# Kernel optimization log

Measured on AMD Instinct MI355X. Metric: run time of the kernel, lower is better.

## Reference

```python
import jax, jax.numpy as jnp
import numpy as np

EPS = 1e-3  # Keras LayerNormalization default epsilon


def setup_inputs() -> dict:
    key = jax.random.key(0)
    ks = jax.random.split(key, 10)
    B, S, D, U = 4, 4096, 1024, 1024
    sc_in = 1.0 / np.sqrt(D)
    sc_u = 1.0 / np.sqrt(U)
    return {
        "inputs": jax.random.normal(ks[0], (B, S, D), dtype=jnp.float32),
        "w1": jax.random.normal(ks[1], (D, U), dtype=jnp.float32) * sc_in,
        "b1": jnp.zeros((U,), dtype=jnp.float32),
        "w2": jax.random.normal(ks[2], (U, U), dtype=jnp.float32) * sc_u,
        "b2": jnp.zeros((U,), dtype=jnp.float32),
        "wg": jax.random.normal(ks[3], (D, U), dtype=jnp.float32) * sc_in,
        "bg": jnp.zeros((U,), dtype=jnp.float32),
        "ws": jax.random.normal(ks[4], (D, U), dtype=jnp.float32) * sc_in,
        "bs": jnp.zeros((U,), dtype=jnp.float32),
        "gamma": jnp.ones((U,), dtype=jnp.float32),
        "beta": jnp.zeros((U,), dtype=jnp.float32),
    }


def reference(inputs, w1, b1, w2, b2, wg, bg, ws, bs, gamma, beta):
    # hidden branch: Dense(relu) -> (dropout inactive at inference) -> Dense
    h = jax.nn.relu(jnp.einsum('bsd,du->bsu', inputs, w1) + b1)
    x = jnp.einsum('bsu,uv->bsv', h, w2) + b2
    # gate on raw inputs
    g = jax.nn.sigmoid(jnp.einsum('bsd,du->bsu', inputs, wg) + bg)
    # skip projection
    s = jnp.einsum('bsd,du->bsu', inputs, ws) + bs
    y = x * g + s
    # LayerNormalization over last axis (Keras default eps=1e-3)
    mu = jnp.mean(y, axis=-1, keepdims=True)
    var = jnp.mean(jnp.square(y - mu), axis=-1, keepdims=True)
    return (y - mu) * jax.lax.rsqrt(var + EPS) * gamma + beta
```

## Files before the change

kernel.cpp:

```cpp
#include <hip/hip_runtime.h>
#include <hip/hip_bf16.h>

typedef short short8 __attribute__((ext_vector_type(8)));
typedef float f32x4 __attribute__((ext_vector_type(4)));

#define M_TOT 16384
#define NDIM  1024
#define BM 256
#define BN 256
#define BK 64
#define KH 32
#define NT (NDIM / BK)

static __device__ __forceinline__ unsigned short f2bf(float f) {
  unsigned int u = __builtin_bit_cast(unsigned int, f);
  unsigned int r = (u + 0x7fffu + ((u >> 16) & 1u)) >> 16;
  return (unsigned short)r;
}
static __device__ __forceinline__ float bf2f(unsigned short u) {
  return __builtin_bit_cast(float, ((unsigned int)u) << 16);
}

__global__ __launch_bounds__(256) void cast_in(const float* __restrict__ in,
                                               unsigned short* __restrict__ out,
                                               int n4) {
  int i = blockIdx.x * 256 + threadIdx.x;
  if (i >= n4) return;
  float4 v = reinterpret_cast<const float4*>(in)[i];
  ushort4 o;
  o.x = f2bf(v.x); o.y = f2bf(v.y); o.z = f2bf(v.z); o.w = f2bf(v.w);
  reinterpret_cast<ushort4*>(out)[i] = o;
}

__global__ __launch_bounds__(256) void tcast(const float* __restrict__ src,
                                             unsigned short* __restrict__ dst) {
  __shared__ unsigned short tile[32][33];
  int bx = blockIdx.x * 32, by = blockIdx.y * 32;
  int x = threadIdx.x & 31, y = threadIdx.x >> 5;
#pragma unroll
  for (int i = 0; i < 32; i += 8)
    tile[y + i][x] = f2bf(src[(size_t)(by + y + i) * NDIM + bx + x]);
  __syncthreads();
#pragma unroll
  for (int i = 0; i < 32; i += 8)
    dst[(size_t)(bx + y + i) * NDIM + by + x] = tile[x][y + i];
}

template <int MODE>
__global__ __launch_bounds__(512, 2) void gemm256(
    const unsigned short* __restrict__ A,
    const unsigned short* __restrict__ Bt,
    const float* __restrict__ bias,
    unsigned short* __restrict__ Obf,
    float* __restrict__ Of,
    const unsigned short* __restrict__ G,
    const float* __restrict__ S) {
  __shared__ __align__(16) unsigned short lds[2][2][2][256][KH];

  const int tid = threadIdx.x;
  const int lane = tid & 63;
  const int wave = tid >> 6;
  const int wm = wave >> 2;
  const int wn = wave & 3;

  const int id = blockIdx.x;
  const int xcd = id & 7;
  const int slot = id >> 3;
  const int rblk = xcd + 8 * (slot >> 2);
  const int cblk = slot & 3;
  const int m0 = rblk * BM, n0 = cblk * BN;

  const unsigned short* gA = A + (size_t)m0 * NDIM;
  const unsigned short* gB = Bt + (size_t)n0 * NDIM;

  f32x4 acc[8][4] = {};

  auto stage = [&](int buf, int mat, int h, const unsigned short* gsrc, int kt) {
#pragma unroll
    for (int j = 0; j < 2; ++j) {
      int cid = j * 512 + tid;
      int row = cid >> 2;
      int cs = cid & 3;
      int c = cs ^ ((row >> 1) & 3);
      const unsigned short* g = gsrc + (size_t)row * NDIM + kt * BK + h * KH + c * 8;
      unsigned short* l = &lds[buf][mat][h][0][0] + (size_t)(j * 512 + (tid & ~63)) * 8;
      __builtin_amdgcn_global_load_lds(
          (__attribute__((address_space(1))) void*)g,
          (__attribute__((address_space(3))) void*)l, 16, 0, 0);
    }
  };

  auto ldA = [&](short8* dst, int buf, int mih, int kk) {
#pragma unroll
    for (int mi = 0; mi < 4; ++mi) {
      int row = wm * 128 + (mih * 4 + mi) * 16 + (lane & 15);
      int cs = (lane >> 4) ^ ((row >> 1) & 3);
      dst[mi] = *reinterpret_cast<const short8*>(&lds[buf][0][kk][row][cs * 8]);
    }
  };
  auto ldB = [&](short8* dst, int buf, int kk) {
#pragma unroll
    for (int nj = 0; nj < 4; ++nj) {
      int row = wn * 64 + nj * 16 + (lane & 15);
      int cs = (lane >> 4) ^ ((row >> 1) & 3);
      dst[nj] = *reinterpret_cast<const short8*>(&lds[buf][1][kk][row][cs * 8]);
    }
  };

#define MFMA_Q(A4, B4, MI0)                                               \
  do {                                                                    \
    _Pragma("unroll") for (int mi = 0; mi < 4; ++mi)                      \
    _Pragma("unroll") for (int nj = 0; nj < 4; ++nj)                      \
      acc[MI0 + mi][nj] = __builtin_amdgcn_mfma_f32_16x16x32_bf16(        \
          A4[mi], B4[nj], acc[MI0 + mi][nj], 0, 0, 0);                    \
  } while (0)

#define PHASE_TAIL()                                          \
  __builtin_amdgcn_s_barrier();                               \
  asm volatile("s_waitcnt lgkmcnt(0)" ::: "memory");          \
  __builtin_amdgcn_sched_barrier(0)

  stage(0, 0, 0, gA, 0);
  stage(0, 1, 0, gB, 0);
  stage(0, 0, 1, gA, 0);
  stage(0, 1, 1, gB, 0);
  asm volatile("s_waitcnt vmcnt(4)" ::: "memory");
  __builtin_amdgcn_s_barrier();

  short8 a_[4], b0_[4], b1_[4];

#pragma unroll 2
  for (int t = 0; t < NT; ++t) {
    const int cur = t & 1, nxt = cur ^ 1;
    const int ktn = (t < NT - 1) ? t + 1 : t;

    stage(nxt, 0, 0, gA, ktn);
    ldA(a_, cur, 0, 0);
    ldB(b0_, cur, 0);
    PHASE_TAIL();
    __builtin_amdgcn_s_setprio(1);
    MFMA_Q(a_, b0_, 0);
    __builtin_amdgcn_s_setprio(0);
    __builtin_amdgcn_s_barrier();

    stage(nxt, 1, 0, gB, ktn);
    ldA(a_, cur, 1, 0);
    PHASE_TAIL();
    __builtin_amdgcn_s_setprio(1);
    MFMA_Q(a_, b0_, 4);
    __builtin_amdgcn_s_setprio(0);
    asm volatile("s_waitcnt vmcnt(4)" ::: "memory");
    __builtin_amdgcn_s_barrier();

    stage(nxt, 0, 1, gA, ktn);
    ldA(a_, cur, 0, 1);
    ldB(b1_, cur, 1);
    PHASE_TAIL();
    __builtin_amdgcn_s_setprio(1);
    MFMA_Q(a_, b1_, 0);
    __builtin_amdgcn_s_setprio(0);
    __builtin_amdgcn_s_barrier();

    stage(nxt, 1, 1, gB, ktn);
    ldA(a_, cur, 1, 1);
    PHASE_TAIL();
    __builtin_amdgcn_s_setprio(1);
    MFMA_Q(a_, b1_, 4);
    __builtin_amdgcn_s_setprio(0);
    asm volatile("s_waitcnt vmcnt(4)" ::: "memory");
    __builtin_amdgcn_s_barrier();
  }

  const int crow0 = m0 + wm * 128;
  const int ccol0 = n0 + wn * 64;
#pragma unroll
  for (int mi = 0; mi < 8; ++mi) {
#pragma unroll
    for (int nj = 0; nj < 4; ++nj) {
      int row = crow0 + mi * 16 + ((lane >> 4) << 2);
      int col = ccol0 + nj * 16 + (lane & 15);
      float bc = bias[col];
#pragma unroll
      for (int r = 0; r < 4; ++r) {
        float v = acc[mi][nj][r] + bc;
        size_t idx = (size_t)(row + r) * NDIM + col;
        if (MODE == 0) {
          Obf[idx] = f2bf(fmaxf(v, 0.f));
        } else if (MODE == 1) {
          Obf[idx] = f2bf(1.f / (1.f + __expf(-v)));
        } else if (MODE == 2) {
          Of[idx] = v;
        } else {
          Of[idx] = v * bf2f(G[idx]) + S[idx];
        }
      }
    }
  }
#undef MFMA_Q
#undef PHASE_TAIL
}

__global__ __launch_bounds__(256) void layernorm_inplace(
    float* __restrict__ Y, const float* __restrict__ gamma,
    const float* __restrict__ beta) {
  const int tid = threadIdx.x;
  float* y = Y + (size_t)blockIdx.x * NDIM;
  float4 v = reinterpret_cast<const float4*>(y)[tid];
  float s1 = v.x + v.y + v.z + v.w;
  float s2 = v.x * v.x + v.y * v.y + v.z * v.z + v.w * v.w;
#pragma unroll
  for (int o = 32; o > 0; o >>= 1) {
    s1 += __shfl_down(s1, o, 64);
    s2 += __shfl_down(s2, o, 64);
  }
  __shared__ float red[8];
  int wave = tid >> 6, lane = tid & 63;
  if (lane == 0) { red[wave] = s1; red[wave + 4] = s2; }
  __syncthreads();
  float S1 = red[0] + red[1] + red[2] + red[3];
  float S2 = red[4] + red[5] + red[6] + red[7];
  float mu = S1 * (1.f / NDIM);
  float var = S2 * (1.f / NDIM) - mu * mu;
  float inv = rsqrtf(var + 1e-3f);
  float4 gm = reinterpret_cast<const float4*>(gamma)[tid];
  float4 bt = reinterpret_cast<const float4*>(beta)[tid];
  float4 o;
  o.x = (v.x - mu) * inv * gm.x + bt.x;
  o.y = (v.y - mu) * inv * gm.y + bt.y;
  o.z = (v.z - mu) * inv * gm.z + bt.z;
  o.w = (v.w - mu) * inv * gm.w + bt.w;
  reinterpret_cast<float4*>(y)[tid] = o;
}

extern "C" void kernel_launch(void* const* d_in, const int* in_sizes, int n_in,
                              void* d_out, int out_size, void* d_ws, size_t ws_size,
                              hipStream_t stream) {
  const float* inp = (const float*)d_in[0];
  const float* w1 = (const float*)d_in[1];
  const float* b1 = (const float*)d_in[2];
  const float* w2 = (const float*)d_in[3];
  const float* b2 = (const float*)d_in[4];
  const float* wg = (const float*)d_in[5];
  const float* bg = (const float*)d_in[6];
  const float* wsk = (const float*)d_in[7];
  const float* bs = (const float*)d_in[8];
  const float* gamma = (const float*)d_in[9];
  const float* beta = (const float*)d_in[10];

  char* p = (char*)d_ws;
  const size_t act_bf16 = (size_t)M_TOT * NDIM * 2;
  const size_t act_f32 = (size_t)M_TOT * NDIM * 4;
  const size_t w_bf16 = (size_t)NDIM * NDIM * 2;
  unsigned short* Ain = (unsigned short*)p; p += act_bf16;
  unsigned short* H   = (unsigned short*)p; p += act_bf16;
  unsigned short* G   = (unsigned short*)p; p += act_bf16;
  float*          S   = (float*)p;          p += act_f32;
  unsigned short* W1t = (unsigned short*)p; p += w_bf16;
  unsigned short* W2t = (unsigned short*)p; p += w_bf16;
  unsigned short* Wgt = (unsigned short*)p; p += w_bf16;
  unsigned short* Wst = (unsigned short*)p; p += w_bf16;
  float* Y = (float*)d_out;

  cast_in<<<(M_TOT * NDIM / 4 + 255) / 256, 256, 0, stream>>>(inp, Ain, M_TOT * NDIM / 4);
  dim3 tg(32, 32);
  tcast<<<tg, 256, 0, stream>>>(w1, W1t);
  tcast<<<tg, 256, 0, stream>>>(w2, W2t);
  tcast<<<tg, 256, 0, stream>>>(wg, Wgt);
  tcast<<<tg, 256, 0, stream>>>(wsk, Wst);

  const int nblk = (M_TOT / BM) * (NDIM / BN);
  gemm256<0><<<nblk, 512, 0, stream>>>(Ain, W1t, b1, H, nullptr, nullptr, nullptr);
  gemm256<1><<<nblk, 512, 0, stream>>>(Ain, Wgt, bg, G, nullptr, nullptr, nullptr);
  gemm256<2><<<nblk, 512, 0, stream>>>(Ain, Wst, bs, nullptr, S, nullptr, nullptr);
  gemm256<3><<<nblk, 512, 0, stream>>>(H, W2t, b2, nullptr, Y, G, S);
  layernorm_inplace<<<M_TOT, 256, 0, stream>>>(Y, gamma, beta);
}
```

Before: 218.0 us.

## Store skip and pre-norm intermediates in bf16 and simplify GEMM phase barriers

```diff
diff --git a/kernel.cpp b/kernel.cpp
--- a/kernel.cpp
+++ b/kernel.cpp
@@ -20,6 +20,8 @@
 static __device__ __forceinline__ float bf2f(unsigned short u) {
   return __builtin_bit_cast(float, ((unsigned int)u) << 16);
 }
+
+#define CLB() asm volatile("" ::: "memory")
 
 __global__ __launch_bounds__(256) void cast_in(const float* __restrict__ in,
                                                unsigned short* __restrict__ out,
@@ -51,10 +53,9 @@
     const unsigned short* __restrict__ A,
     const unsigned short* __restrict__ Bt,
     const float* __restrict__ bias,
-    unsigned short* __restrict__ Obf,
-    float* __restrict__ Of,
+    unsigned short* __restrict__ O,
     const unsigned short* __restrict__ G,
-    const float* __restrict__ S) {
+    const unsigned short* __restrict__ S) {
   __shared__ __align__(16) unsigned short lds[2][2][2][256][KH];
 
   const int tid = threadIdx.x;
@@ -115,17 +116,14 @@
           A4[mi], B4[nj], acc[MI0 + mi][nj], 0, 0, 0);                    \
   } while (0)
 
-#define PHASE_TAIL()                                          \
-  __builtin_amdgcn_s_barrier();                               \
-  asm volatile("s_waitcnt lgkmcnt(0)" ::: "memory");          \
-  __builtin_amdgcn_sched_barrier(0)
+#define BAR() do { CLB(); __builtin_amdgcn_s_barrier(); CLB(); } while (0)
 
   stage(0, 0, 0, gA, 0);
   stage(0, 1, 0, gB, 0);
   stage(0, 0, 1, gA, 0);
   stage(0, 1, 1, gB, 0);
   asm volatile("s_waitcnt vmcnt(4)" ::: "memory");
-  __builtin_amdgcn_s_barrier();
+  BAR();
 
   short8 a_[4], b0_[4], b1_[4];
 
@@ -137,38 +135,38 @@
     stage(nxt, 0, 0, gA, ktn);
     ldA(a_, cur, 0, 0);
     ldB(b0_, cur, 0);
-    PHASE_TAIL();
+    BAR();
     __builtin_amdgcn_s_setprio(1);
     MFMA_Q(a_, b0_, 0);
     __builtin_amdgcn_s_setprio(0);
-    __builtin_amdgcn_s_barrier();
+    BAR();
 
     stage(nxt, 1, 0, gB, ktn);
     ldA(a_, cur, 1, 0);
-    PHASE_TAIL();
+    BAR();
     __builtin_amdgcn_s_setprio(1);
     MFMA_Q(a_, b0_, 4);
     __builtin_amdgcn_s_setprio(0);
     asm volatile("s_waitcnt vmcnt(4)" ::: "memory");
-    __builtin_amdgcn_s_barrier();
+    BAR();
 
     stage(nxt, 0, 1, gA, ktn);
     ldA(a_, cur, 0, 1);
     ldB(b1_, cur, 1);
-    PHASE_TAIL();
+    BAR();
     __builtin_amdgcn_s_setprio(1);
     MFMA_Q(a_, b1_, 0);
     __builtin_amdgcn_s_setprio(0);
-    __builtin_amdgcn_s_barrier();
+    BAR();
 
     stage(nxt, 1, 1, gB, ktn);
     ldA(a_, cur, 1, 1);
-    PHASE_TAIL();
+    BAR();
     __builtin_amdgcn_s_setprio(1);
     MFMA_Q(a_, b1_, 4);
     __builtin_amdgcn_s_setprio(0);
     asm volatile("s_waitcnt vmcnt(4)" ::: "memory");
-    __builtin_amdgcn_s_barrier();
+    BAR();
   }
 
   const int crow0 = m0 + wm * 128;
@@ -185,29 +183,30 @@
         float v = acc[mi][nj][r] + bc;
         size_t idx = (size_t)(row + r) * NDIM + col;
         if (MODE == 0) {
-          Obf[idx] = f2bf(fmaxf(v, 0.f));
+          O[idx] = f2bf(fmaxf(v, 0.f));
         } else if (MODE == 1) {
-          Obf[idx] = f2bf(1.f / (1.f + __expf(-v)));
+          O[idx] = f2bf(1.f / (1.f + __expf(-v)));
         } else if (MODE == 2) {
-          Of[idx] = v;
+          O[idx] = f2bf(v);
         } else {
-          Of[idx] = v * bf2f(G[idx]) + S[idx];
+          O[idx] = f2bf(v * bf2f(G[idx]) + bf2f(S[idx]));
         }
       }
     }
   }
 #undef MFMA_Q
-#undef PHASE_TAIL
-}
-
-__global__ __launch_bounds__(256) void layernorm_inplace(
-    float* __restrict__ Y, const float* __restrict__ gamma,
-    const float* __restrict__ beta) {
+#undef BAR
+}
+
+__global__ __launch_bounds__(256) void layernorm_bf(
+    const unsigned short* __restrict__ Ybf, float* __restrict__ Out,
+    const float* __restrict__ gamma, const float* __restrict__ beta) {
   const int tid = threadIdx.x;
-  float* y = Y + (size_t)blockIdx.x * NDIM;
-  float4 v = reinterpret_cast<const float4*>(y)[tid];
-  float s1 = v.x + v.y + v.z + v.w;
-  float s2 = v.x * v.x + v.y * v.y + v.z * v.z + v.w * v.w;
+  const unsigned short* y = Ybf + (size_t)blockIdx.x * NDIM;
+  ushort4 u = reinterpret_cast<const ushort4*>(y)[tid];
+  float v0 = bf2f(u.x), v1 = bf2f(u.y), v2 = bf2f(u.z), v3 = bf2f(u.w);
+  float s1 = v0 + v1 + v2 + v3;
+  float s2 = v0 * v0 + v1 * v1 + v2 * v2 + v3 * v3;
 #pragma unroll
   for (int o = 32; o > 0; o >>= 1) {
     s1 += __shfl_down(s1, o, 64);
@@ -225,11 +224,11 @@
   float4 gm = reinterpret_cast<const float4*>(gamma)[tid];
   float4 bt = reinterpret_cast<const float4*>(beta)[tid];
   float4 o;
-  o.x = (v.x - mu) * inv * gm.x + bt.x;
-  o.y = (v.y - mu) * inv * gm.y + bt.y;
-  o.z = (v.z - mu) * inv * gm.z + bt.z;
-  o.w = (v.w - mu) * inv * gm.w + bt.w;
-  reinterpret_cast<float4*>(y)[tid] = o;
+  o.x = (v0 - mu) * inv * gm.x + bt.x;
+  o.y = (v1 - mu) * inv * gm.y + bt.y;
+  o.z = (v2 - mu) * inv * gm.z + bt.z;
+  o.w = (v3 - mu) * inv * gm.w + bt.w;
+  reinterpret_cast<float4*>(Out + (size_t)blockIdx.x * NDIM)[tid] = o;
 }
 
 extern "C" void kernel_launch(void* const* d_in, const int* in_sizes, int n_in,
@@ -249,17 +248,16 @@
 
   char* p = (char*)d_ws;
   const size_t act_bf16 = (size_t)M_TOT * NDIM * 2;
-  const size_t act_f32 = (size_t)M_TOT * NDIM * 4;
   const size_t w_bf16 = (size_t)NDIM * NDIM * 2;
   unsigned short* Ain = (unsigned short*)p; p += act_bf16;
   unsigned short* H   = (unsigned short*)p; p += act_bf16;
   unsigned short* G   = (unsigned short*)p; p += act_bf16;
-  float*          S   = (float*)p;          p += act_f32;
+  unsigned short* S   = (unsigned short*)p; p += act_bf16;
+  unsigned short* Ybf = (unsigned short*)p; p += act_bf16;
   unsigned short* W1t = (unsigned short*)p; p += w_bf16;
   unsigned short* W2t = (unsigned short*)p; p += w_bf16;
   unsigned short* Wgt = (unsigned short*)p; p += w_bf16;
   unsigned short* Wst = (unsigned short*)p; p += w_bf16;
-  float* Y = (float*)d_out;
 
   cast_in<<<(M_TOT * NDIM / 4 + 255) / 256, 256, 0, stream>>>(inp, Ain, M_TOT * NDIM / 4);
   dim3 tg(32, 32);
@@ -269,9 +267,9 @@
   tcast<<<tg, 256, 0, stream>>>(wsk, Wst);
 
   const int nblk = (M_TOT / BM) * (NDIM / BN);
-  gemm256<0><<<nblk, 512, 0, stream>>>(Ain, W1t, b1, H, nullptr, nullptr, nullptr);
-  gemm256<1><<<nblk, 512, 0, stream>>>(Ain, Wgt, bg, G, nullptr, nullptr, nullptr);
-  gemm256<2><<<nblk, 512, 0, stream>>>(Ain, Wst, bs, nullptr, S, nullptr, nullptr);
-  gemm256<3><<<nblk, 512, 0, stream>>>(H, W2t, b2, nullptr, Y, G, S);
-  layernorm_inplace<<<M_TOT, 256, 0, stream>>>(Y, gamma, beta);
-}
+  gemm256<0><<<nblk, 512, 0, stream>>>(Ain, W1t, b1, H, nullptr, nullptr);
+  gemm256<1><<<nblk, 512, 0, stream>>>(Ain, Wgt, bg, G, nullptr, nullptr);
+  gemm256<2><<<nblk, 512, 0, stream>>>(Ain, Wst, bs, S, nullptr, nullptr);
+  gemm256<3><<<nblk, 512, 0, stream>>>(H, W2t, b2, Ybf, G, S);
+  layernorm_bf<<<M_TOT, 256, 0, stream>>>(Ybf, (float*)d_out, gamma, beta);
+}
```

After: 207.2 us. 4.9% less time.
